# Optimization experiments

Hardware: AMD Instinct MI355X
Metric: run time of the kernel (lower is better)

## Reference

```python
import jax, jax.numpy as jnp
import numpy as np

EPS = 1e-06


def setup_inputs() -> dict:
    key = jax.random.key(0)
    k1, k2 = jax.random.split(key)
    B, T, E = 4, 4096, 1024
    M = E // 2
    x = jax.random.normal(k1, (B, T, E), dtype=jnp.float32)
    # causal mask: position i may attend to j <= i... note module multiplies K
    # (which is nonzero only for j >= i) by mask; a standard causal lower-tri
    # mask would zero everything but the diagonal. The module's bump kernel
    # looks FORWARD (diff = (j-i).clamp(min=0)), so the natural mask here is
    # upper-triangular (j >= i), i.e. the 'causal' mask for this pooling.
    mask = jnp.triu(jnp.ones((T, T), dtype=bool))
    gate_raw = jnp.full((M,), -3.0, dtype=jnp.float32)
    return {"x": x, "mask": mask, "gate_raw": gate_raw}


def reference(x, mask, gate_raw):
    B, T, E = x.shape
    dtype = x.dtype
    x_c = x[..., 0::2]                                  # (B, T, M) content channels

    # convex bump kernel K[i, j], nonzero for j >= i
    i = jnp.arange(T, dtype=dtype)[:, None]
    j = jnp.arange(T, dtype=dtype)[None, :]
    diff = jnp.maximum(j - i, 0.0)
    horizon = jnp.maximum(jnp.float32(T) - i, 1.0)
    u = jnp.minimum(diff / horizon, 1.0 - EPS)
    K = jnp.exp(1.0 - 1.0 / (1.0 - u * u + EPS))
    K = jnp.where(u >= 1.0 - EPS, jnp.asarray(EPS, dtype), K)

    K = K * mask.astype(dtype)
    K = K / jnp.maximum(K.sum(-1, keepdims=True), EPS)  # row-normalize

    phi = jnp.einsum('ij,bjm->bim', K, x_c)             # (B, T, M)
    gate = jax.nn.softplus(gate_raw)[None, None, :]     # (1, 1, M)
    out = x.at[..., 1::2].set(phi * gate)               # write phase channels
    return out
```

## Files before the change

### kernel.cpp

```cpp
#include <hip/hip_runtime.h>
#include <cstdint>
#include <cstddef>

#define Tdim 4096
#define Bdim 4
#define Edim 1024
#define Mdim 512
#define EPSF 1e-6f
#define NTILES 1056

typedef __bf16 bf16x8 __attribute__((ext_vector_type(8)));
typedef float f32x4 __attribute__((ext_vector_type(4)));

__host__ __device__ __forceinline__ int panel_start(int p) { return p * (65 - p); }

__device__ __forceinline__ unsigned short f2bf(float f) {
  union { float f; unsigned int u; } a; a.f = f;
  unsigned int r = a.u + 0x7fffu + ((a.u >> 16) & 1u);
  return (unsigned short)(r >> 16);
}

__device__ __forceinline__ unsigned int pack_bf16(float a, float b) {
  union { float f; unsigned int u; } ua, ub; ua.f = a; ub.f = b;
  return __builtin_amdgcn_perm(ub.u + 0x8000u, ua.u + 0x8000u, 0x07060302u);
}

__device__ __forceinline__ float kernel_g(float dj, float inv_h) {
  float u = fminf(dj * inv_h, 1.0f - EPSF);
  return __expf(1.0f - 1.0f / (1.0f - u * u + EPSF));
}

typedef void __attribute__((address_space(1)))* gas1;
typedef void __attribute__((address_space(3)))* las3;
__device__ __forceinline__ void load_lds16(const void* g, void* l) {
  __builtin_amdgcn_global_load_lds((gas1)(g), (las3)(l), 16, 0, 0);
}

__global__ __launch_bounds__(256) void prep_kernel(const float* __restrict__ x,
                                                   float* __restrict__ inv_s,
                                                   unsigned short* __restrict__ XcT) {
  __shared__ float smem[1104];
  const int tid = threadIdx.x;
  const int id = blockIdx.x;
  if (id < Tdim) {
    const int i = id;
    const float inv_h = __fdividef(1.0f, (float)(Tdim - i));
    float s = 0.0f;
    for (int j = i + tid; j < Tdim; j += 256)
      s += kernel_g((float)(j - i), inv_h);
#pragma unroll
    for (int off = 32; off; off >>= 1) s += __shfl_down(s, off);
    if ((tid & 63) == 0) smem[1088 + (tid >> 6)] = s;
    __syncthreads();
    if (tid == 0)
      inv_s[i] = __fdividef(
          1.0f, fmaxf(smem[1088] + smem[1089] + smem[1090] + smem[1091], EPSF));
  } else {
    const int eid = id - Tdim;
    const int j0 = (eid & 63) * 64;
    const int m0 = ((eid >> 6) & 15) * 32;
    const int b  = eid >> 10;
    unsigned short* Ls = reinterpret_cast<unsigned short*>(smem);
    const int q = tid & 15;
    const int jbase = tid >> 4;
#pragma unroll
    for (int it = 0; it < 4; ++it) {
      const int jj = jbase + it * 16;
      const size_t off = ((size_t)(b * Tdim + j0 + jj)) * Edim + 2 * m0 + 4 * q;
      const float4 v = *reinterpret_cast<const float4*>(&x[off]);
      Ls[(2 * q) * 68 + jj]     = f2bf(v.x);
      Ls[(2 * q + 1) * 68 + jj] = f2bf(v.z);
    }
    __syncthreads();
    const int ch = tid & 15;
    const int mb = tid >> 4;
#pragma unroll
    for (int it = 0; it < 2; ++it) {
      const int m = mb + it * 16;
      ushort4 uv;
      uv.x = Ls[m * 68 + 4 * ch];
      uv.y = Ls[m * 68 + 4 * ch + 1];
      uv.z = Ls[m * 68 + 4 * ch + 2];
      uv.w = Ls[m * 68 + 4 * ch + 3];
      *reinterpret_cast<ushort4*>(
          &XcT[((size_t)(b * Mdim + m0 + m)) * Tdim + j0 + 4 * ch]) = uv;
    }
  }
}

__global__ __launch_bounds__(256) void packK_kernel(const float* __restrict__ inv_s,
                                                    unsigned short* __restrict__ Kswz) {
  const int id = blockIdx.x;
  int p = 0;
  while (id >= (p + 1) * (64 - p)) ++p;
  const int jt = id - panel_start(p);
  const int i0 = p * 128;
  const int jb0 = i0 + jt * 64;
  unsigned short* dst = Kswz + (size_t)id * 8192;
  const int tid = threadIdx.x;
#pragma unroll
  for (int ss = 0; ss < 4; ++ss) {
    const int G = ss * 256 + tid;
    const int lane = G & 63;
    const int kk = (G >> 6) & 1;
    const int r  = (G >> 7) & 3;
    const int h  = G >> 9;
    const int li = h * 64 + r * 16 + (lane & 15);
    const int i  = i0 + li;
    const float inv_h = __fdividef(1.0f, (float)(Tdim - i));
    const float sinv = inv_s[i];
    const int jb = jb0 + (kk * 4 + (lane >> 4)) * 8;
    float v[8];
#pragma unroll
    for (int e = 0; e < 8; ++e) {
      const int j = jb + e;
      v[e] = (j >= i) ? kernel_g((float)(j - i), inv_h) * sinv : 0.0f;
    }
    uint4 pk;
    pk.x = pack_bf16(v[0], v[1]);
    pk.y = pack_bf16(v[2], v[3]);
    pk.z = pack_bf16(v[4], v[5]);
    pk.w = pack_bf16(v[6], v[7]);
    *reinterpret_cast<uint4*>(&dst[(size_t)G * 8]) = pk;
  }
}

__global__ __launch_bounds__(256) void gemm_kernel(
    const unsigned short* __restrict__ Kswz,
    const unsigned short* __restrict__ XcT,
    const float* __restrict__ x,
    const float* __restrict__ graw,
    float* __restrict__ out) {
  __shared__ unsigned short Bs[3][128 * 64];
  const int id = blockIdx.x;
  int p;
  if (id < 256) p = id >> 4;
  else          p = 31 - ((id - 256) >> 4);
  const int mb = id & 15;
  const int i0 = p * 128;
  const int m0 = (mb & 3) * 128;
  const int b  = mb >> 2;
  const int tid = threadIdx.x;
  const int w = tid >> 6;
  const int l = tid & 63;
  const int wr = w >> 1, wc = w & 1;
  const unsigned short* Brow = XcT + ((size_t)b * Mdim + m0) * Tdim;
  const int srow  = l >> 3;
  const int sslot = l & 7;
  const int schunk = (sslot ^ srow) * 8;
  const unsigned short* Apan =
      Kswz + (size_t)panel_start(p) * 8192 + (size_t)(wr * 8) * 512 + (size_t)l * 8;

  f32x4 acc[4][4] = {};
  const int n = (Tdim - i0) >> 6;
  const int lr16 = l & 15;
  const int kq = l >> 4;

#pragma unroll
  for (int q = 0; q < 4; ++q) {
    const int rr = (w * 4 + q) * 8 + srow;
    load_lds16(Brow + (size_t)rr * Tdim + (i0 + schunk), &Bs[0][(w * 4 + q) * 512]);
  }
  asm volatile("" ::: "memory");
  bf16x8 af0[2][4], af1[2][4];
#pragma unroll
  for (int r = 0; r < 4; ++r) {
    af0[0][r] = *reinterpret_cast<const bf16x8*>(Apan + (r * 2 + 0) * 512);
    af0[1][r] = *reinterpret_cast<const bf16x8*>(Apan + (r * 2 + 1) * 512);
  }
  asm volatile("" ::: "memory");
#pragma unroll
  for (int q = 0; q < 4; ++q) {
    const int rr = (w * 4 + q) * 8 + srow;
    load_lds16(Brow + (size_t)rr * Tdim + (i0 + 64 + schunk), &Bs[1][(w * 4 + q) * 512]);
  }

#define GHALF(tc, afC, afN)                                                       \
  do {                                                                            \
    asm volatile("s_waitcnt vmcnt(12)" ::: "memory");                             \
    __builtin_amdgcn_s_barrier();                                                 \
    __builtin_amdgcn_sched_barrier(0);                                            \
                       \
    const int tpre = ((tc) + 1 < n) ? (tc) + 1 : n - 1;                           \
    const unsigned short* Ap = Apan + (size_t)tpre * 8192;                        \
    _Pragma("unroll")                                                             \
    for (int r = 0; r < 4; ++r) {                                                 \
      afN[0][r] = *reinterpret_cast<const bf16x8*>(Ap + (r * 2 + 0) * 512);       \
      afN[1][r] = *reinterpret_cast<const bf16x8*>(Ap + (r * 2 + 1) * 512);       \
    }                                                                             \
              \
    {                                                                             \
      const int ts = (tc) + 2;                                                    \
      const int jn = i0 + (((ts) < n) ? (ts) : n - 1) * 64;                       \
      unsigned short* bdst = Bs[(ts) % 3];                                        \
      _Pragma("unroll")                                                           \
      for (int q = 0; q < 4; ++q) {                                               \
        const int rr = (w * 4 + q) * 8 + srow;                                    \
        load_lds16(Brow + (size_t)rr * Tdim + (jn + schunk),                      \
                   &bdst[(w * 4 + q) * 512]);                                     \
      }                                                                           \
    }                                                                             \
                                         \
    {                                                                             \
      const unsigned short* bsrc = Bs[(tc) % 3];                                  \
      _Pragma("unroll")                                                           \
      for (int kk = 0; kk < 2; ++kk) {                                            \
        bf16x8 bfr[4];                                                            \
        const int chunk = kk * 4 + kq;                                            \
        const int slot = (chunk ^ (lr16 & 7)) * 8;                \
        _Pragma("unroll")                                                         \
        for (int c = 0; c < 4; ++c)                                               \
          bfr[c] = *reinterpret_cast<const bf16x8*>(                              \
              &bsrc[(wc * 64 + c * 16 + lr16) * 64 + slot]);                      \
        _Pragma("unroll")                                                         \
        for (int r = 0; r < 4; ++r)                                               \
          _Pragma("unroll")                                                       \
          for (int c = 0; c < 4; ++c)                                             \
            acc[r][c] = __builtin_amdgcn_mfma_f32_16x16x32_bf16(                  \
                afC[kk][r], bfr[c], acc[r][c], 0, 0, 0);                          \
      }                                                                           \
    }                                                                             \
  } while (0)

  for (int t = 0; t < n; t += 2) {
    GHALF(t, af0, af1);
    GHALF(t + 1, af1, af0);
  }
#undef GHALF

  const int lr = l & 15;
  const int lq = l >> 4;
  float gm[4];
#pragma unroll
  for (int c = 0; c < 4; ++c) {
    const float v = graw[m0 + wc * 64 + c * 16 + lr];
    gm[c] = fmaxf(v, 0.0f) + __logf(1.0f + __expf(-fabsf(v)));
  }
#pragma unroll
  for (int r = 0; r < 4; ++r) {
    const int ii = i0 + wr * 64 + r * 16 + lq * 4;
#pragma unroll
    for (int c = 0; c < 4; ++c) {
      const int m = m0 + wc * 64 + c * 16 + lr;
#pragma unroll
      for (int v = 0; v < 4; ++v) {
        const size_t o = ((size_t)(b * Tdim + ii + v)) * Edim + 2 * m;
        const float2 xv = *reinterpret_cast<const float2*>(&x[o]);
        float2 res;
        res.x = xv.x;
        res.y = acc[r][c][v] * gm[c];
        *reinterpret_cast<float2*>(&out[o]) = res;
      }
    }
  }
}

__global__ __launch_bounds__(256) void fallback_kernel(const float* __restrict__ x,
                                                       const float* __restrict__ graw,
                                                       float* __restrict__ out) {
  const int i = blockIdx.x, b = blockIdx.y, tid = threadIdx.x;
  const float inv_h = 1.0f / (float)(Tdim - i);
  float s = 0.0f;
  for (int j = i + tid; j < Tdim; j += 256)
    s += kernel_g((float)(j - i), inv_h);
#pragma unroll
  for (int off = 32; off; off >>= 1) s += __shfl_down(s, off);
  __shared__ float red[4];
  __shared__ float sinv_sh;
  if ((tid & 63) == 0) red[tid >> 6] = s;
  __syncthreads();
  if (tid == 0) sinv_sh = 1.0f / (red[0] + red[1] + red[2] + red[3]);
  __syncthreads();
  const float sinv = sinv_sh;
  const float* xb = x + (size_t)b * Tdim * Edim;
  float a0 = 0.0f, a1 = 0.0f;
  const int m0 = tid, m1 = tid + 256;
  for (int j = i; j < Tdim; ++j) {
    const float wgt = kernel_g((float)(j - i), inv_h);
    const float* xr = xb + (size_t)j * Edim;
    a0 += wgt * xr[2 * m0];
    a1 += wgt * xr[2 * m1];
  }
  const float v0 = graw[m0], v1 = graw[m1];
  const float g0 = fmaxf(v0, 0.0f) + log1pf(__expf(-fabsf(v0)));
  const float g1 = fmaxf(v1, 0.0f) + log1pf(__expf(-fabsf(v1)));
  const size_t o = ((size_t)(b * Tdim + i)) * Edim;
  const float* xi = xb + (size_t)i * Edim;
  out[o + 2 * m0]     = xi[2 * m0];
  out[o + 2 * m0 + 1] = a0 * sinv * g0;
  out[o + 2 * m1]     = xi[2 * m1];
  out[o + 2 * m1 + 1] = a1 * sinv * g1;
}

extern "C" void kernel_launch(void* const* d_in, const int* in_sizes, int n_in,
                              void* d_out, int out_size, void* d_ws, size_t ws_size,
                              hipStream_t stream) {
  const float* x = (const float*)d_in[0];
  const float* gate_raw = (const float*)d_in[2];
  float* out = (float*)d_out;

  const size_t XcT_bytes  = (size_t)Bdim * Mdim * Tdim * 2;
  const size_t Kswz_bytes = (size_t)NTILES * 16384;
  const size_t inv_bytes  = (size_t)Tdim * 4;
  const size_t need = XcT_bytes + Kswz_bytes + inv_bytes;

  if (ws_size < need) {
    fallback_kernel<<<dim3(Tdim, Bdim), 256, 0, stream>>>(x, gate_raw, out);
    return;
  }

  char* ws = (char*)d_ws;
  unsigned short* XcT  = (unsigned short*)ws;
  unsigned short* Kswz = (unsigned short*)(ws + XcT_bytes);
  float* inv_s         = (float*)(ws + XcT_bytes + Kswz_bytes);

  prep_kernel<<<dim3(2 * Tdim), 256, 0, stream>>>(x, inv_s, XcT);
  packK_kernel<<<dim3(NTILES), 256, 0, stream>>>(inv_s, Kswz);
  gemm_kernel<<<dim3(512), 256, 0, stream>>>(Kswz, XcT, x, gate_raw, out);
}
```

Baseline: 221.6 us.

## Split GEMM K-loop across two wave groups with LDS reduction

```diff
diff --git a/kernel.cpp b/kernel.cpp
--- a/kernel.cpp
+++ b/kernel.cpp
@@ -125,13 +125,13 @@
   }
 }
 
-__global__ __launch_bounds__(256) void gemm_kernel(
+__global__ __launch_bounds__(512, 4) void gemm_kernel(
     const unsigned short* __restrict__ Kswz,
     const unsigned short* __restrict__ XcT,
     const float* __restrict__ x,
     const float* __restrict__ graw,
     float* __restrict__ out) {
-  __shared__ unsigned short Bs[3][128 * 64];
+  __shared__ unsigned short Bs[2][2][128 * 64];
   const int id = blockIdx.x;
   int p;
   if (id < 256) p = id >> 4;
@@ -142,8 +142,10 @@
   const int b  = mb >> 2;
   const int tid = threadIdx.x;
   const int w = tid >> 6;
+  const int grp = w >> 2;
+  const int wl = w & 3;
   const int l = tid & 63;
-  const int wr = w >> 1, wc = w & 1;
+  const int wr = wl >> 1, wc = wl & 1;
   const unsigned short* Brow = XcT + ((size_t)b * Mdim + m0) * Tdim;
   const int srow  = l >> 3;
   const int sslot = l & 7;
@@ -153,56 +155,56 @@
 
   f32x4 acc[4][4] = {};
   const int n = (Tdim - i0) >> 6;
+  const int nh = n >> 1;
+  const int tbase = grp * nh;
   const int lr16 = l & 15;
   const int kq = l >> 4;
 
 #pragma unroll
   for (int q = 0; q < 4; ++q) {
-    const int rr = (w * 4 + q) * 8 + srow;
-    load_lds16(Brow + (size_t)rr * Tdim + (i0 + schunk), &Bs[0][(w * 4 + q) * 512]);
+    const int rr = (wl * 4 + q) * 8 + srow;
+    load_lds16(Brow + (size_t)rr * Tdim + (i0 + tbase * 64 + schunk),
+               &Bs[grp][0][(wl * 4 + q) * 512]);
   }
   asm volatile("" ::: "memory");
   bf16x8 af0[2][4], af1[2][4];
 #pragma unroll
   for (int r = 0; r < 4; ++r) {
-    af0[0][r] = *reinterpret_cast<const bf16x8*>(Apan + (r * 2 + 0) * 512);
-    af0[1][r] = *reinterpret_cast<const bf16x8*>(Apan + (r * 2 + 1) * 512);
+    af0[0][r] = *reinterpret_cast<const bf16x8*>(Apan + (size_t)tbase * 8192 + (r * 2 + 0) * 512);
+    af0[1][r] = *reinterpret_cast<const bf16x8*>(Apan + (size_t)tbase * 8192 + (r * 2 + 1) * 512);
   }
   asm volatile("" ::: "memory");
-#pragma unroll
-  for (int q = 0; q < 4; ++q) {
-    const int rr = (w * 4 + q) * 8 + srow;
-    load_lds16(Brow + (size_t)rr * Tdim + (i0 + 64 + schunk), &Bs[1][(w * 4 + q) * 512]);
-  }
 
 #define GHALF(tc, afC, afN)                                                       \
   do {                                                                            \
-    asm volatile("s_waitcnt vmcnt(12)" ::: "memory");                             \
+    asm volatile("s_waitcnt vmcnt(8)" ::: "memory");                              \
     __builtin_amdgcn_s_barrier();                                                 \
     __builtin_amdgcn_sched_barrier(0);                                            \
-                       \
-    const int tpre = ((tc) + 1 < n) ? (tc) + 1 : n - 1;                           \
-    const unsigned short* Ap = Apan + (size_t)tpre * 8192;                        \
-    _Pragma("unroll")                                                             \
-    for (int r = 0; r < 4; ++r) {                                                 \
-      afN[0][r] = *reinterpret_cast<const bf16x8*>(Ap + (r * 2 + 0) * 512);       \
-      afN[1][r] = *reinterpret_cast<const bf16x8*>(Ap + (r * 2 + 1) * 512);       \
-    }                                                                             \
               \
     {                                                                             \
-      const int ts = (tc) + 2;                                                    \
-      const int jn = i0 + (((ts) < n) ? (ts) : n - 1) * 64;                       \
-      unsigned short* bdst = Bs[(ts) % 3];                                        \
+      const int ts = (tc) + 1;                                                    \
+      const int tt = tbase + ((ts < nh) ? ts : nh - 1);                           \
+      unsigned short* bdst = Bs[grp][ts & 1];                                     \
       _Pragma("unroll")                                                           \
       for (int q = 0; q < 4; ++q) {                                               \
-        const int rr = (w * 4 + q) * 8 + srow;                                    \
-        load_lds16(Brow + (size_t)rr * Tdim + (jn + schunk),                      \
-                   &bdst[(w * 4 + q) * 512]);                                     \
+        const int rr = (wl * 4 + q) * 8 + srow;                                   \
+        load_lds16(Brow + (size_t)rr * Tdim + (i0 + tt * 64 + schunk),            \
+                   &bdst[(wl * 4 + q) * 512]);                                    \
       }                                                                           \
     }                                                                             \
-                                         \
+                       \
     {                                                                             \
-      const unsigned short* bsrc = Bs[(tc) % 3];                                  \
+      const int tpre = tbase + (((tc) + 1 < nh) ? (tc) + 1 : nh - 1);             \
+      const unsigned short* Ap = Apan + (size_t)tpre * 8192;                      \
+      _Pragma("unroll")                                                           \
+      for (int r = 0; r < 4; ++r) {                                               \
+        afN[0][r] = *reinterpret_cast<const bf16x8*>(Ap + (r * 2 + 0) * 512);     \
+        afN[1][r] = *reinterpret_cast<const bf16x8*>(Ap + (r * 2 + 1) * 512);     \
+      }                                                                           \
+    }                                                                             \
+                                    \
+    {                                                                             \
+      const unsigned short* bsrc = Bs[grp][(tc) & 1];                             \
       _Pragma("unroll")                                                           \
       for (int kk = 0; kk < 2; ++kk) {                                            \
         bf16x8 bfr[4];                                                            \
@@ -222,34 +224,61 @@
     }                                                                             \
   } while (0)
 
-  for (int t = 0; t < n; t += 2) {
+  for (int t = 0; t + 1 < nh; t += 2) {
     GHALF(t, af0, af1);
     GHALF(t + 1, af1, af0);
   }
+  if (nh & 1) GHALF(nh - 1, af0, af1);
 #undef GHALF
 
-  const int lr = l & 15;
-  const int lq = l >> 4;
-  float gm[4];
-#pragma unroll
-  for (int c = 0; c < 4; ++c) {
-    const float v = graw[m0 + wc * 64 + c * 16 + lr];
-    gm[c] = fmaxf(v, 0.0f) + __logf(1.0f + __expf(-fabsf(v)));
-  }
-#pragma unroll
-  for (int r = 0; r < 4; ++r) {
-    const int ii = i0 + wr * 64 + r * 16 + lq * 4;
+  __syncthreads();
+  float* Cb = reinterpret_cast<float*>(&Bs[0][0][0]);
+  const int tig = wl * 64 + l;
+  if (grp == 1) {
+#pragma unroll
+    for (int r = 0; r < 4; ++r)
+#pragma unroll
+      for (int c = 0; c < 4; ++c) {
+        const int cc = r * 4 + c;
+        const int slot = tig * 16 + (cc ^ (tig & 15));
+        *reinterpret_cast<f32x4*>(&Cb[slot * 4]) = acc[r][c];
+      }
+  }
+  __syncthreads();
+  if (grp == 0) {
+#pragma unroll
+    for (int r = 0; r < 4; ++r)
+#pragma unroll
+      for (int c = 0; c < 4; ++c) {
+        const int cc = r * 4 + c;
+        const int slot = tig * 16 + (cc ^ (tig & 15));
+        const f32x4 part = *reinterpret_cast<const f32x4*>(&Cb[slot * 4]);
+        acc[r][c] += part;
+      }
+
+    const int lr = l & 15;
+    const int lq = l >> 4;
+    float gm[4];
 #pragma unroll
     for (int c = 0; c < 4; ++c) {
-      const int m = m0 + wc * 64 + c * 16 + lr;
-#pragma unroll
-      for (int v = 0; v < 4; ++v) {
-        const size_t o = ((size_t)(b * Tdim + ii + v)) * Edim + 2 * m;
-        const float2 xv = *reinterpret_cast<const float2*>(&x[o]);
-        float2 res;
-        res.x = xv.x;
-        res.y = acc[r][c][v] * gm[c];
-        *reinterpret_cast<float2*>(&out[o]) = res;
+      const float v = graw[m0 + wc * 64 + c * 16 + lr];
+      gm[c] = fmaxf(v, 0.0f) + __logf(1.0f + __expf(-fabsf(v)));
+    }
+#pragma unroll
+    for (int r = 0; r < 4; ++r) {
+      const int ii = i0 + wr * 64 + r * 16 + lq * 4;
+#pragma unroll
+      for (int c = 0; c < 4; ++c) {
+        const int m = m0 + wc * 64 + c * 16 + lr;
+#pragma unroll
+        for (int v = 0; v < 4; ++v) {
+          const size_t o = ((size_t)(b * Tdim + ii + v)) * Edim + 2 * m;
+          const float2 xv = *reinterpret_cast<const float2*>(&x[o]);
+          float2 res;
+          res.x = xv.x;
+          res.y = acc[r][c][v] * gm[c];
+          *reinterpret_cast<float2*>(&out[o]) = res;
+        }
       }
     }
   }
@@ -316,5 +345,5 @@
 
   prep_kernel<<<dim3(2 * Tdim), 256, 0, stream>>>(x, inv_s, XcT);
   packK_kernel<<<dim3(NTILES), 256, 0, stream>>>(inv_s, Kswz);
-  gemm_kernel<<<dim3(512), 256, 0, stream>>>(Kswz, XcT, x, gate_raw, out);
-}
+  gemm_kernel<<<dim3(512), 512, 0, stream>>>(Kswz, XcT, x, gate_raw, out);
+}
```

After: 293.4 us. 1.32x slower.
